# Kernel tuning notes

Measured on AMD Instinct MI355X. Metric: run time of the kernel, lower is better.

The kernel has to match this reference:

```python
import jax, jax.numpy as jnp
import numpy as np
from jax import lax

NEG = -1e9  # stand-in for -inf that keeps gradients finite
T, V, L = 2048, 32000, 8


def setup_inputs() -> dict:
    key = jax.random.key(0)
    k1, k2, k3 = jax.random.split(key, 3)
    # log piece probabilities (valid distribution in log space)
    log_piece_probs = jax.nn.log_softmax(jax.random.normal(k1, (V,), dtype=jnp.float32))
    # match_idx[t, j] = vocab index of the (unique) piece matching sequence[t:t+j+1], or -1
    match_idx = jax.random.randint(k2, (T, L), 0, V, dtype=jnp.int32)
    keep = jax.random.uniform(k3, (T, L)) < 0.3
    keep = keep.at[:, 0].set(True)  # length-1 (single char) pieces always match -> segmentable
    in_range = (jnp.arange(T)[:, None] + jnp.arange(1, L + 1)[None, :]) <= T
    match_idx = jnp.where(keep & in_range, match_idx, -1)
    return {"log_piece_probs": log_piece_probs, "match_idx": match_idx}


def _forward(log_piece_probs, match_idx):
    T_, L_ = match_idx.shape
    V_ = log_piece_probs.shape[0]
    valid = match_idx >= 0
    # w[t, j] = log p(piece matching at pos t with length j+1), NEG if no match
    w = jnp.where(valid, log_piece_probs[jnp.clip(match_idx, 0)], NEG)  # [T, L]
    # wrev[r, j] = w[r - j, j]: contribution ending at position n = r+1 from length j+1
    wrev = jnp.stack(
        [jnp.pad(w[:, j], (j, 0), constant_values=NEG)[:T_] for j in range(L_)], axis=1
    )  # [T, L]

    # forward pass: alpha[n] = logsumexp_l alpha[n-l] + w[n-l, l-1], rolling buffer of last L alphas
    def astep(buf, wr):
        a = jax.nn.logsumexp(buf[::-1] + wr)  # buf[::-1][j] = alpha[n-1-j]
        return jnp.concatenate([buf[1:], a[None]]), a

    abuf0 = jnp.concatenate([jnp.full((L_ - 1,), NEG, jnp.float32), jnp.zeros((1,), jnp.float32)])
    _, a_rest = lax.scan(astep, abuf0, wrev)
    alpha = jnp.concatenate([jnp.zeros((1,), jnp.float32), a_rest])  # [T+1], alpha[0]=0

    # backward pass: beta[t] = logsumexp_l w[t, l-1] + beta[t+l], rolling buffer of next L betas
    def bstep(buf, wt):
        b = jax.nn.logsumexp(wt + buf)  # buf[j] = beta[t+1+j]
        return jnp.concatenate([b[None], buf[:-1]]), b

    bbuf0 = jnp.concatenate([jnp.zeros((1,), jnp.float32), jnp.full((L_ - 1,), NEG, jnp.float32)])
    _, b_rest = lax.scan(bstep, bbuf0, w, reverse=True)
    beta = jnp.concatenate([b_rest, jnp.zeros((1,), jnp.float32)])  # [T+1], beta[T]=0

    # posterior: P[t, i] = exp(alpha[t] + log p_i + beta[t+len] - alpha[T])
    nxt = jnp.arange(T_)[:, None] + jnp.arange(1, L_ + 1)[None, :]  # [T, L]
    beta_next = beta[jnp.clip(nxt, 0, T_)]
    logP = alpha[:T_, None] + w + beta_next - alpha[T_]
    vals = jnp.where(valid, jnp.exp(logP), 0.0)  # [T, L]
    P = jnp.zeros((T_, V_), jnp.float32).at[
        jnp.arange(T_)[:, None], jnp.clip(match_idx, 0)
    ].add(vals)
    return P


def reference(log_piece_probs, match_idx):
    return _forward(log_piece_probs, match_idx)
```

## Files before the change

kernel.cpp:

```cpp
#include <hip/hip_runtime.h>


#define NEGV -1e9f
constexpr int T = 2048;
constexpr int L = 8;
constexpr int V = 32000;
constexpr int NCH = 32;
constexpr int K = 64;
constexpr int GRID = 2048;

__device__ __forceinline__ float lse8v(float t0, float t1, float t2, float t3,
                                       float t4, float t5, float t6, float t7) {
    float m = fmaxf(fmaxf(fmaxf(t0, t1), fmaxf(t2, t3)),
                    fmaxf(fmaxf(t4, t5), fmaxf(t6, t7)));
    float s = __expf(t0 - m) + __expf(t1 - m) + __expf(t2 - m) + __expf(t3 - m)
            + __expf(t4 - m) + __expf(t5 - m) + __expf(t6 - m) + __expf(t7 - m);
    return m + __logf(s);
}

__device__ void chunked_scan(const float* __restrict__ w, float* __restrict__ Pm,
                             float* __restrict__ vst, float* __restrict__ outv,
                             bool backward) {
    const int tid = threadIdx.x;

    {
        const int c = tid >> 3, col = tid & 7;
        float q[8];
#pragma unroll
        for (int i = 0; i < 8; ++i) q[i] = (i == col) ? 0.f : NEGV;
        const float4* wr4 = (const float4*)(w + c * K * 8);
        float4 c0 = wr4[0], c1 = wr4[1];
        float4 b0 = wr4[2], b1 = wr4[3];
        for (int k = 0; k < K; ++k) {
            float4 a0, a1;
            if (k + 2 < K) { a0 = wr4[(k + 2) * 2]; a1 = wr4[(k + 2) * 2 + 1]; }
            float top = lse8v(c0.x + q[0], c0.y + q[1], c0.z + q[2], c0.w + q[3],
                              c1.x + q[4], c1.y + q[5], c1.z + q[6], c1.w + q[7]);
#pragma unroll
            for (int i = 7; i > 0; --i) q[i] = q[i - 1];
            q[0] = top;
            c0 = b0; c1 = b1; b0 = a0; b1 = a1;
        }
#pragma unroll
        for (int i = 0; i < 8; ++i) Pm[c * 64 + i * 8 + col] = q[i];
    }
    __syncthreads();

    if (tid < 8) {
        const int r = tid;
        float v = (r == 0) ? 0.f : NEGV;
        float4 r0 = ((const float4*)(Pm + r * 8))[0];
        float4 r1 = ((const float4*)(Pm + r * 8))[1];
        for (int cc = 0; cc < NCH; ++cc) {
            vst[cc * 8 + r] = v;
            float4 n0, n1;
            if (cc + 1 < NCH) {
                n0 = ((const float4*)(Pm + (cc + 1) * 64 + r * 8))[0];
                n1 = ((const float4*)(Pm + (cc + 1) * 64 + r * 8))[1];
            }
            float vb0 = __shfl(v, 0, 8), vb1 = __shfl(v, 1, 8);
            float vb2 = __shfl(v, 2, 8), vb3 = __shfl(v, 3, 8);
            float vb4 = __shfl(v, 4, 8), vb5 = __shfl(v, 5, 8);
            float vb6 = __shfl(v, 6, 8), vb7 = __shfl(v, 7, 8);
            v = lse8v(r0.x + vb0, r0.y + vb1, r0.z + vb2, r0.w + vb3,
                      r1.x + vb4, r1.y + vb5, r1.z + vb6, r1.w + vb7);
            r0 = n0; r1 = n1;
        }
        vst[NCH * 8 + r] = v;
    }
    __syncthreads();

    if (tid < NCH) {
        const int cc = tid;
        float ab[8];
#pragma unroll
        for (int i = 0; i < 8; ++i) ab[i] = vst[cc * 8 + i];
        const float4* wr4 = (const float4*)(w + cc * K * 8);
        float4 c0 = wr4[0], c1 = wr4[1];
        float4 b0 = wr4[2], b1 = wr4[3];
        for (int k = 0; k < K; ++k) {
            float4 a0, a1;
            if (k + 2 < K) { a0 = wr4[(k + 2) * 2]; a1 = wr4[(k + 2) * 2 + 1]; }
            float val = lse8v(c0.x + ab[0], c0.y + ab[1], c0.z + ab[2], c0.w + ab[3],
                              c1.x + ab[4], c1.y + ab[5], c1.z + ab[6], c1.w + ab[7]);
            int s = cc * K + k;
            if (!backward) outv[s + 1] = val;
            else           outv[T - 1 - s] = val;
#pragma unroll
            for (int i = 7; i > 0; --i) ab[i] = ab[i - 1];
            ab[0] = val;
            c0 = b0; c1 = b1; b0 = a0; b1 = a1;
        }
    }
}

__global__ __launch_bounds__(256) void scan_fill_kernel(
        const float* __restrict__ logp, const int* __restrict__ midx,
        float* __restrict__ out, float* __restrict__ alpha, float* __restrict__ beta,
        float* __restrict__ wf, float* __restrict__ wb,
        float* __restrict__ Pmf, float* __restrict__ Pmb,
        float* __restrict__ vstf, float* __restrict__ vstb) {
    const int tid = threadIdx.x;

    if (blockIdx.x == 0) {
        for (int o = tid; o < T * L; o += 256) {
            int r = o >> 3, j = o & 7, t = r - j;
            float v = NEGV;
            if (t >= 0) { int m = midx[t * 8 + j]; if (m >= 0) v = logp[m]; }
            wf[o] = v;
        }
        if (tid == 0) alpha[0] = 0.f;
        __syncthreads();
        chunked_scan(wf, Pmf, vstf, alpha, false);
    } else if (blockIdx.x == 1) {
        for (int o = tid; o < T * L; o += 256) {
            int s = o >> 3, j = o & 7, t = T - 1 - s;
            int m = midx[t * 8 + j];
            wb[o] = (m >= 0) ? logp[m] : NEGV;
        }
        if (tid == 0) beta[T] = 0.f;
        __syncthreads();
        chunked_scan(wb, Pmb, vstb, beta, true);
    } else {
        float4 z = make_float4(0.f, 0.f, 0.f, 0.f);
        float4* o4 = (float4*)out;
        const size_t n4 = (size_t)T * V / 4;
        size_t i = (size_t)(blockIdx.x - 2) * blockDim.x + tid;
        const size_t stride = (size_t)(GRID - 2) * blockDim.x;
        for (; i < n4; i += stride) o4[i] = z;
    }
}

__global__ __launch_bounds__(256) void scatter_kernel(
        const float* __restrict__ logp, const int* __restrict__ midx,
        float* __restrict__ out, const float* __restrict__ alpha,
        const float* __restrict__ beta) {
    int i = blockIdx.x * blockDim.x + threadIdx.x;
    if (i >= T * L) return;
    int m = midx[i];
    if (m < 0) return;
    int t = i >> 3, j = i & 7;
    int nx = t + j + 1;
    if (nx > T) nx = T;
    float lp = alpha[t] + logp[m] + beta[nx] - alpha[T];
    atomicAdd(&out[(size_t)t * V + m], __expf(lp));
}

extern "C" void kernel_launch(void* const* d_in, const int* in_sizes, int n_in,
                              void* d_out, int out_size, void* d_ws, size_t ws_size,
                              hipStream_t stream) {
    const float* logp = (const float*)d_in[0];
    const int*   midx = (const int*)d_in[1];
    float* out = (float*)d_out;

    float* ws    = (float*)d_ws;
    float* alpha = ws;
    float* beta  = alpha + 2064;
    float* wf    = beta + 2064;
    float* wb    = wf + 16384;
    float* Pmf   = wb + 16384;
    float* Pmb   = Pmf + 2048;
    float* vstf  = Pmb + 2048;
    float* vstb  = vstf + 272;

    scan_fill_kernel<<<dim3(GRID), 256, 0, stream>>>(logp, midx, out, alpha, beta,
                                                     wf, wb, Pmf, Pmb, vstf, vstb);
    scatter_kernel<<<dim3((T * L) / 256), 256, 0, stream>>>(logp, midx, out, alpha, beta);
}
```

Before: 341.0 us.

## Retile scan chunks, move scan scratch to LDS, use exp2/log2, nontemporal zero fill

```diff
diff --git a/kernel.cpp b/kernel.cpp
--- a/kernel.cpp
+++ b/kernel.cpp
@@ -2,26 +2,69 @@
 
 
 #define NEGV -1e9f
+#define LOG2E 1.4426950408889634f
 constexpr int T = 2048;
 constexpr int L = 8;
 constexpr int V = 32000;
-constexpr int NCH = 32;
-constexpr int K = 64;
-constexpr int GRID = 2048;
+constexpr int NCH = 64;
+constexpr int K = 32;
+constexpr int BLK = 512;
+constexpr int FILLB = 4096;
+constexpr int N4 = T * V / 4;
+constexpr int CH4 = N4 / FILLB;
+
+typedef float vfloat4 __attribute__((ext_vector_type(4)));
+
+__device__ __forceinline__ float hexp2(float x) { return __builtin_amdgcn_exp2f(x); }
+__device__ __forceinline__ float hlog2(float x) { return __builtin_amdgcn_logf(x); }
 
 __device__ __forceinline__ float lse8v(float t0, float t1, float t2, float t3,
                                        float t4, float t5, float t6, float t7) {
     float m = fmaxf(fmaxf(fmaxf(t0, t1), fmaxf(t2, t3)),
                     fmaxf(fmaxf(t4, t5), fmaxf(t6, t7)));
-    float s = __expf(t0 - m) + __expf(t1 - m) + __expf(t2 - m) + __expf(t3 - m)
-            + __expf(t4 - m) + __expf(t5 - m) + __expf(t6 - m) + __expf(t7 - m);
-    return m + __logf(s);
+    float s = hexp2(t0 - m) + hexp2(t1 - m) + hexp2(t2 - m) + hexp2(t3 - m)
+            + hexp2(t4 - m) + hexp2(t5 - m) + hexp2(t6 - m) + hexp2(t7 - m);
+    return m + hlog2(s);
 }
 
-__device__ void chunked_scan(const float* __restrict__ w, float* __restrict__ Pm,
-                             float* __restrict__ vst, float* __restrict__ outv,
-                             bool backward) {
+__global__ __launch_bounds__(BLK) void scan_fill_kernel(
+        const float* __restrict__ logp, const int* __restrict__ midx,
+        float* __restrict__ out, float* __restrict__ alpha, float* __restrict__ beta,
+        float* __restrict__ wf, float* __restrict__ wb) {
     const int tid = threadIdx.x;
+    const int bx = blockIdx.x;
+
+    if (bx >= 2) {
+        vfloat4 z = (vfloat4)0.f;
+        vfloat4* o4 = (vfloat4*)out;
+        const int base4 = (bx - 2) * CH4;
+        const int end4 = base4 + CH4;
+        for (int i = base4 + tid; i < end4; i += BLK)
+            __builtin_nontemporal_store(z, &o4[i]);
+        return;
+    }
+
+    __shared__ __align__(16) float sPm[NCH * 64];
+    __shared__ float sVst[(NCH + 1) * 8];
+
+    float* w = (bx == 0) ? wf : wb;
+    if (bx == 0) {
+        for (int o = tid; o < T * L; o += BLK) {
+            int r = o >> 3, j = o & 7, t = r - j;
+            float v = NEGV;
+            if (t >= 0) { int m = midx[(t << 3) + j]; if (m >= 0) v = logp[m] * LOG2E; }
+            wf[o] = v;
+        }
+        if (tid == 0) alpha[0] = 0.f;
+    } else {
+        for (int o = tid; o < T * L; o += BLK) {
+            int s = o >> 3, j = o & 7, t = T - 1 - s;
+            int m = midx[(t << 3) + j];
+            wb[o] = (m >= 0) ? logp[m] * LOG2E : NEGV;
+        }
+        if (tid == 0) beta[T] = 0.f;
+    }
+    __syncthreads();
 
     {
         const int c = tid >> 3, col = tid & 7;
@@ -42,31 +85,25 @@
             c0 = b0; c1 = b1; b0 = a0; b1 = a1;
         }
 #pragma unroll
-        for (int i = 0; i < 8; ++i) Pm[c * 64 + i * 8 + col] = q[i];
+        for (int i = 0; i < 8; ++i) sPm[c * 64 + i * 8 + col] = q[i];
     }
     __syncthreads();
 
     if (tid < 8) {
         const int r = tid;
         float v = (r == 0) ? 0.f : NEGV;
-        float4 r0 = ((const float4*)(Pm + r * 8))[0];
-        float4 r1 = ((const float4*)(Pm + r * 8))[1];
         for (int cc = 0; cc < NCH; ++cc) {
-            vst[cc * 8 + r] = v;
-            float4 n0, n1;
-            if (cc + 1 < NCH) {
-                n0 = ((const float4*)(Pm + (cc + 1) * 64 + r * 8))[0];
-                n1 = ((const float4*)(Pm + (cc + 1) * 64 + r * 8))[1];
-            }
+            sVst[cc * 8 + r] = v;
+            float4 r0 = *(const float4*)&sPm[cc * 64 + r * 8];
+            float4 r1 = *(const float4*)&sPm[cc * 64 + r * 8 + 4];
             float vb0 = __shfl(v, 0, 8), vb1 = __shfl(v, 1, 8);
             float vb2 = __shfl(v, 2, 8), vb3 = __shfl(v, 3, 8);
             float vb4 = __shfl(v, 4, 8), vb5 = __shfl(v, 5, 8);
             float vb6 = __shfl(v, 6, 8), vb7 = __shfl(v, 7, 8);
             v = lse8v(r0.x + vb0, r0.y + vb1, r0.z + vb2, r0.w + vb3,
                       r1.x + vb4, r1.y + vb5, r1.z + vb6, r1.w + vb7);
-            r0 = n0; r1 = n1;
         }
-        vst[NCH * 8 + r] = v;
+        sVst[NCH * 8 + r] = v;
     }
     __syncthreads();
 
@@ -74,7 +111,7 @@
         const int cc = tid;
         float ab[8];
 #pragma unroll
-        for (int i = 0; i < 8; ++i) ab[i] = vst[cc * 8 + i];
+        for (int i = 0; i < 8; ++i) ab[i] = sVst[cc * 8 + i];
         const float4* wr4 = (const float4*)(w + cc * K * 8);
         float4 c0 = wr4[0], c1 = wr4[1];
         float4 b0 = wr4[2], b1 = wr4[3];
@@ -84,50 +121,13 @@
             float val = lse8v(c0.x + ab[0], c0.y + ab[1], c0.z + ab[2], c0.w + ab[3],
                               c1.x + ab[4], c1.y + ab[5], c1.z + ab[6], c1.w + ab[7]);
             int s = cc * K + k;
-            if (!backward) outv[s + 1] = val;
-            else           outv[T - 1 - s] = val;
+            if (bx == 0) alpha[s + 1] = val;
+            else         beta[T - 1 - s] = val;
 #pragma unroll
             for (int i = 7; i > 0; --i) ab[i] = ab[i - 1];
             ab[0] = val;
             c0 = b0; c1 = b1; b0 = a0; b1 = a1;
         }
-    }
-}
-
-__global__ __launch_bounds__(256) void scan_fill_kernel(
-        const float* __restrict__ logp, const int* __restrict__ midx,
-        float* __restrict__ out, float* __restrict__ alpha, float* __restrict__ beta,
-        float* __restrict__ wf, float* __restrict__ wb,
-        float* __restrict__ Pmf, float* __restrict__ Pmb,
-        float* __restrict__ vstf, float* __restrict__ vstb) {
-    const int tid = threadIdx.x;
-
-    if (blockIdx.x == 0) {
-        for (int o = tid; o < T * L; o += 256) {
-            int r = o >> 3, j = o & 7, t = r - j;
-            float v = NEGV;
-            if (t >= 0) { int m = midx[t * 8 + j]; if (m >= 0) v = logp[m]; }
-            wf[o] = v;
-        }
-        if (tid == 0) alpha[0] = 0.f;
-        __syncthreads();
-        chunked_scan(wf, Pmf, vstf, alpha, false);
-    } else if (blockIdx.x == 1) {
-        for (int o = tid; o < T * L; o += 256) {
-            int s = o >> 3, j = o & 7, t = T - 1 - s;
-            int m = midx[t * 8 + j];
-            wb[o] = (m >= 0) ? logp[m] : NEGV;
-        }
-        if (tid == 0) beta[T] = 0.f;
-        __syncthreads();
-        chunked_scan(wb, Pmb, vstb, beta, true);
-    } else {
-        float4 z = make_float4(0.f, 0.f, 0.f, 0.f);
-        float4* o4 = (float4*)out;
-        const size_t n4 = (size_t)T * V / 4;
-        size_t i = (size_t)(blockIdx.x - 2) * blockDim.x + tid;
-        const size_t stride = (size_t)(GRID - 2) * blockDim.x;
-        for (; i < n4; i += stride) o4[i] = z;
     }
 }
 
@@ -142,8 +142,8 @@
     int t = i >> 3, j = i & 7;
     int nx = t + j + 1;
     if (nx > T) nx = T;
-    float lp = alpha[t] + logp[m] + beta[nx] - alpha[T];
-    atomicAdd(&out[(size_t)t * V + m], __expf(lp));
+    float lp2 = alpha[t] + logp[m] * LOG2E + beta[nx] - alpha[T];
+    atomicAdd(&out[(size_t)t * V + m], hexp2(lp2));
 }
 
 extern "C" void kernel_launch(void* const* d_in, const int* in_sizes, int n_in,
@@ -158,12 +158,7 @@
     float* beta  = alpha + 2064;
     float* wf    = beta + 2064;
     float* wb    = wf + 16384;
-    float* Pmf   = wb + 16384;
-    float* Pmb   = Pmf + 2048;
-    float* vstf  = Pmb + 2048;
-    float* vstb  = vstf + 272;
 
-    scan_fill_kernel<<<dim3(GRID), 256, 0, stream>>>(logp, midx, out, alpha, beta,
-                                                     wf, wb, Pmf, Pmb, vstf, vstb);
+    scan_fill_kernel<<<dim3(2 + FILLB), BLK, 0, stream>>>(logp, midx, out, alpha, beta, wf, wb);
     scatter_kernel<<<dim3((T * L) / 256), 256, 0, stream>>>(logp, midx, out, alpha, beta);
 }
```

After: 310.9 us. -8.8%, faster.
